# Kernel optimization log

Measured on AMD Instinct MI355X. Metric: run time of the kernel, lower is better.

The kernel has to match this reference:

```python
import jax, jax.numpy as jnp
import numpy as np

N_NODES = 50000
N_EDGES = 1_000_000
N_HYPER = 1024
F_IN = 128
F_EDGE = 64


def setup_inputs() -> dict:
    key = jax.random.key(0)
    ks = jax.random.split(key, 20)
    s = 0.05
    return {
        "x": jax.random.normal(ks[0], (N_NODES, F_IN), jnp.float32),
        "edge_index": jax.random.randint(ks[1], (2, N_EDGES), 0, N_NODES, dtype=jnp.int64),
        "edge_weight": jax.random.uniform(ks[2], (N_EDGES,), jnp.float32),
        "edge_features": jax.random.normal(ks[3], (N_HYPER, F_EDGE), jnp.float32),
        "adj_e": jax.random.uniform(ks[4], (N_HYPER, N_HYPER), jnp.float32) / N_HYPER,
        "T": jax.random.uniform(ks[5], (N_NODES, N_HYPER), jnp.float32) / N_HYPER,
        # HypergraphConvLayer 1: 128 -> 64
        "W1": jax.random.normal(ks[6], (F_IN, 64), jnp.float32) * s,
        "b1": jnp.zeros((64,), jnp.float32),
        # HypergraphConvLayer 2: 64 -> 32
        "W2": jax.random.normal(ks[7], (64, 32), jnp.float32) * s,
        "b2": jnp.zeros((32,), jnp.float32),
        # GraphConvolution (CensNet-style): node 32->32, edge 64->32
        "Wn": jax.random.normal(ks[8], (32, 32), jnp.float32) * s,
        "We": jax.random.normal(ks[9], (F_EDGE, 32), jnp.float32) * s,
        "bg": jnp.zeros((32,), jnp.float32),
        # class_classifier: Linear(32,32) -> ReLU -> Linear(32,2) -> Softmax
        "Wc1": jax.random.normal(ks[10], (32, 32), jnp.float32) * s,
        "bc1": jnp.zeros((32,), jnp.float32),
        "Wc2": jax.random.normal(ks[11], (32, 2), jnp.float32) * s,
        "bc2": jnp.zeros((2,), jnp.float32),
    }


def _hconv(h, W, b, src, dst, edge_weight, num_nodes):
    # linear projection then edge-weighted scatter-add: out[dst] += w * h[src]
    h = h @ W + b
    msg = h[src] * edge_weight[:, None]          # [E, d]
    return jax.ops.segment_sum(msg, dst, num_segments=num_nodes)


def reference(x, edge_index, edge_weight, edge_features, adj_e, T,
              W1, b1, W2, b2, Wn, We, bg, Wc1, bc1, Wc2, bc2):
    n = x.shape[0]
    src, dst = edge_index[0], edge_index[1]

    h = jax.nn.relu(_hconv(x, W1, b1, src, dst, edge_weight, n))   # [N,64]
    h = jax.nn.relu(_hconv(h, W2, b2, src, dst, edge_weight, n))   # [N,32]

    # aggregate_node_features: node_features[dst] += h[src]; / num_edges
    num_edges = edge_index.shape[1]
    node_features = jax.ops.segment_sum(h[src], dst, num_segments=n) / num_edges

    # edge_conv: node linear + incidence-weighted hyperedge convolution
    edge_h = adj_e @ (edge_features @ We)                           # [NE,32]
    shared = jax.nn.relu(node_features @ Wn + T @ edge_h + bg)      # [N,32]

    # class_classifier
    c = jax.nn.relu(shared @ Wc1 + bc1)
    logits = c @ Wc2 + bc2
    return jax.nn.softmax(logits, axis=1)                           # [N,2]
```

## Files before the change

### kernel.cpp

```cpp
#include <hip/hip_runtime.h>
#include <hip/hip_bf16.h>

#define RPB 256

template<int COLS, int K>
__global__ __launch_bounds__(256) void gemm_k(
    const float* __restrict__ X, const float* __restrict__ W,
    const float* __restrict__ bias, float* __restrict__ out,
    int nrows, float scale, int relu_in)
{
    constexpr int CPT = COLS / 8;
    constexpr int KT  = 32;
    constexpr int NKT = K / KT;

    __shared__ float sx[RPB * 36];
    __shared__ float sWT[COLS * 33];

    const int tid = threadIdx.x;
    const int cg  = tid & 7;
    const int rg  = tid >> 3;
    const int r0  = blockIdx.x * RPB;

    float acc[8][CPT];
    #pragma unroll
    for (int r = 0; r < 8; ++r)
        #pragma unroll
        for (int c = 0; c < CPT; ++c) acc[r][c] = 0.f;

    for (int kt = 0; kt < NKT; ++kt) {
        #pragma unroll
        for (int j = 0; j < 8; ++j) {
            int i  = tid + j * 256;
            int r  = i >> 3;
            int k4 = i & 7;
            int gr = r0 + r; if (gr >= nrows) gr = nrows - 1;
            float4 v = *(const float4*)&X[(size_t)gr * K + kt * KT + k4 * 4];
            if (relu_in) {
                v.x = fmaxf(v.x, 0.f); v.y = fmaxf(v.y, 0.f);
                v.z = fmaxf(v.z, 0.f); v.w = fmaxf(v.w, 0.f);
            }
            if (scale != 1.f) { v.x *= scale; v.y *= scale; v.z *= scale; v.w *= scale; }
            *(float4*)&sx[r * 36 + k4 * 4] = v;
        }
        for (int i = tid; i < COLS * KT; i += 256) {
            int kl = i / COLS, c = i % COLS;
            sWT[c * 33 + kl] = W[(size_t)(kt * KT + kl) * COLS + c];
        }
        __syncthreads();

        #pragma unroll
        for (int k4 = 0; k4 < 8; ++k4) {
            float4 a[8];
            #pragma unroll
            for (int r = 0; r < 8; ++r)
                a[r] = *(const float4*)&sx[(r * 32 + rg) * 36 + k4 * 4];
            #pragma unroll
            for (int cc = 0; cc < CPT; ++cc) {
                int c = cg * CPT + cc;
                float w0 = sWT[c * 33 + k4 * 4 + 0];
                float w1 = sWT[c * 33 + k4 * 4 + 1];
                float w2 = sWT[c * 33 + k4 * 4 + 2];
                float w3 = sWT[c * 33 + k4 * 4 + 3];
                #pragma unroll
                for (int r = 0; r < 8; ++r)
                    acc[r][cc] += a[r].x * w0 + a[r].y * w1 + a[r].z * w2 + a[r].w * w3;
            }
        }
        __syncthreads();
    }

    #pragma unroll
    for (int r = 0; r < 8; ++r) {
        int row = r0 + r * 32 + rg;
        if (row < nrows) {
            #pragma unroll
            for (int cc4 = 0; cc4 < CPT / 4; ++cc4) {
                int c = cg * CPT + cc4 * 4;
                float4 o;
                o.x = acc[r][cc4 * 4 + 0] + (bias ? bias[c + 0] : 0.f);
                o.y = acc[r][cc4 * 4 + 1] + (bias ? bias[c + 1] : 0.f);
                o.z = acc[r][cc4 * 4 + 2] + (bias ? bias[c + 2] : 0.f);
                o.w = acc[r][cc4 * 4 + 3] + (bias ? bias[c + 3] : 0.f);
                *(float4*)&out[(size_t)row * COLS + c] = o;
            }
        }
    }
}

__global__ __launch_bounds__(256, 4) void tgemm2_k(
    const float* __restrict__ T, const float* __restrict__ eh,
    float* __restrict__ par, int nrows)
{
    __shared__ float seh[256 * 32];
    const int tid = threadIdx.x;
    const int ks  = blockIdx.y * 256;

    #pragma unroll
    for (int j = 0; j < 8; ++j) {
        int i = tid + j * 256;
        *(float4*)&seh[i * 4] = *(const float4*)&eh[(size_t)ks * 32 + (size_t)i * 4];
    }
    __syncthreads();

    int row = blockIdx.x * 256 + tid;
    int r   = row < nrows ? row : nrows - 1;
    const float* Tp = T + (size_t)r * 1024 + ks;

    float acc[32];
    #pragma unroll
    for (int c = 0; c < 32; ++c) acc[c] = 0.f;

    float4 t[8];
    #pragma unroll
    for (int q = 0; q < 8; ++q) t[q] = *(const float4*)&Tp[q * 4];

    for (int kc = 0; kc < 8; ++kc) {
        float4 tn[8];
        if (kc < 7) {
            #pragma unroll
            for (int q = 0; q < 8; ++q)
                tn[q] = *(const float4*)&Tp[(kc + 1) * 32 + q * 4];
        }
        #pragma unroll
        for (int q = 0; q < 8; ++q) {
            #pragma unroll
            for (int j = 0; j < 4; ++j) {
                float a = (j == 0) ? t[q].x : (j == 1) ? t[q].y : (j == 2) ? t[q].z : t[q].w;
                int k = kc * 32 + q * 4 + j;
                #pragma unroll
                for (int c4 = 0; c4 < 8; ++c4) {
                    float4 w = *(const float4*)&seh[k * 32 + c4 * 4];
                    acc[c4 * 4 + 0] += a * w.x;
                    acc[c4 * 4 + 1] += a * w.y;
                    acc[c4 * 4 + 2] += a * w.z;
                    acc[c4 * 4 + 3] += a * w.w;
                }
            }
        }
        #pragma unroll
        for (int q = 0; q < 8; ++q) t[q] = tn[q];
    }

    if (row < nrows) {
        float* p = par + (size_t)blockIdx.y * nrows * 32 + (size_t)row * 32;
        #pragma unroll
        for (int c4 = 0; c4 < 8; ++c4)
            *(float4*)&p[c4 * 4] = make_float4(acc[c4 * 4 + 0], acc[c4 * 4 + 1],
                                               acc[c4 * 4 + 2], acc[c4 * 4 + 3]);
    }
}

__global__ __launch_bounds__(256) void classify_k(
    const float* __restrict__ par, const float* __restrict__ nfw,
    const float* __restrict__ bg, const float* __restrict__ Wc1,
    const float* __restrict__ bc1, const float* __restrict__ Wc2,
    const float* __restrict__ bc2, float* __restrict__ out, int nrows)
{
    __shared__ float sWc1T[1024];
    __shared__ float sWc2[64];
    __shared__ float sb[66];

    int tid = threadIdx.x;
    for (int i = tid; i < 1024; i += 256)
        sWc1T[(i & 31) * 32 + (i >> 5)] = Wc1[i];
    if (tid < 64) sWc2[tid] = Wc2[tid];
    if (tid < 32)      sb[tid] = bc1[tid];
    else if (tid < 64) sb[tid] = bg[tid - 32];
    else if (tid < 66) sb[tid] = bc2[tid - 64];
    __syncthreads();

    int row = blockIdx.x * 256 + tid;
    if (row >= nrows) return;

    size_t stride = (size_t)nrows * 32;
    float4 sh4[8];
    #pragma unroll
    for (int i4 = 0; i4 < 8; ++i4) {
        const float* base = par + (size_t)row * 32 + i4 * 4;
        float4 v0 = *(const float4*)(base);
        float4 v1 = *(const float4*)(base + stride);
        float4 v2 = *(const float4*)(base + 2 * stride);
        float4 v3 = *(const float4*)(base + 3 * stride);
        float4 nf = *(const float4*)&nfw[(size_t)row * 32 + i4 * 4];
        float4 o;
        o.x = fmaxf(v0.x + v1.x + v2.x + v3.x + nf.x + sb[32 + i4 * 4 + 0], 0.f);
        o.y = fmaxf(v0.y + v1.y + v2.y + v3.y + nf.y + sb[32 + i4 * 4 + 1], 0.f);
        o.z = fmaxf(v0.z + v1.z + v2.z + v3.z + nf.z + sb[32 + i4 * 4 + 2], 0.f);
        o.w = fmaxf(v0.w + v1.w + v2.w + v3.w + nf.w + sb[32 + i4 * 4 + 3], 0.f);
        sh4[i4] = o;
    }

    float l0 = sb[64], l1 = sb[65];
    #pragma unroll
    for (int jj = 0; jj < 32; ++jj) {
        float s = sb[jj];
        #pragma unroll
        for (int i4 = 0; i4 < 8; ++i4) {
            float4 w4 = *(const float4*)&sWc1T[jj * 32 + i4 * 4];
            s += sh4[i4].x * w4.x + sh4[i4].y * w4.y
               + sh4[i4].z * w4.z + sh4[i4].w * w4.w;
        }
        s = fmaxf(s, 0.f);
        l0 += s * sWc2[jj * 2 + 0];
        l1 += s * sWc2[jj * 2 + 1];
    }
    float p0 = 1.f / (1.f + expf(l1 - l0));
    float p1 = 1.f / (1.f + expf(l0 - l1));
    *(float2*)&out[(size_t)row * 2] = make_float2(p0, p1);
}

__global__ void hist_k(const int* __restrict__ dst, int* __restrict__ deg, int E)
{
    int e = blockIdx.x * 256 + threadIdx.x;
    if (e < E) atomicAdd(&deg[dst[e]], 1);
}

__global__ void scan1_k(const int* __restrict__ deg, int* __restrict__ bsum, int N)
{
    __shared__ int s[256];
    int t = threadIdx.x, i = blockIdx.x * 256 + t;
    s[t] = (i < N) ? deg[i] : 0;
    __syncthreads();
    for (int off = 128; off > 0; off >>= 1) {
        if (t < off) s[t] += s[t + off];
        __syncthreads();
    }
    if (t == 0) bsum[blockIdx.x] = s[0];
}

__global__ void scan2_k(const int* __restrict__ bsum, int* __restrict__ boff,
                        int NB, int* __restrict__ rsN)
{
    __shared__ int s[256];
    int t = threadIdx.x;
    int v = (t < NB) ? bsum[t] : 0;
    s[t] = v;
    __syncthreads();
    for (int off = 1; off < 256; off <<= 1) {
        int u = (t >= off) ? s[t - off] : 0;
        __syncthreads();
        s[t] += u;
        __syncthreads();
    }
    if (t < NB) boff[t] = s[t] - v;
    if (t == NB - 1) *rsN = s[t];
}

__global__ void scan3_k(const int* __restrict__ deg, const int* __restrict__ boff,
                        int* __restrict__ rs, int* __restrict__ cur, int N)
{
    __shared__ int s[256];
    int t = threadIdx.x, i = blockIdx.x * 256 + t;
    int v = (i < N) ? deg[i] : 0;
    s[t] = v;
    __syncthreads();
    for (int off = 1; off < 256; off <<= 1) {
        int u = (t >= off) ? s[t - off] : 0;
        __syncthreads();
        s[t] += u;
        __syncthreads();
    }
    if (i < N) {
        int ex = boff[blockIdx.x] + s[t] - v;
        rs[i] = ex;
        cur[i] = ex;
    }
}

__global__ void fill_k(const int* __restrict__ src, const int* __restrict__ dst,
                       const float* __restrict__ ew, int* __restrict__ cur,
                       int2* __restrict__ epk, int E)
{
    int e = blockIdx.x * 256 + threadIdx.x;
    if (e < E) {
        int pos = atomicAdd(&cur[dst[e]], 1);
        epk[pos] = make_int2(src[e], __float_as_int(ew[e]));
    }
}

__global__ __launch_bounds__(256) void gather64_k(
    const float* __restrict__ hp, const int2* __restrict__ epk,
    const int* __restrict__ rs, float* __restrict__ outv, int N)
{
    int t = blockIdx.x * 256 + threadIdx.x;
    if (t >= N * 16) return;
    int n  = t >> 4;
    int ch = t & 15;
    int j0 = rs[n], j1 = rs[n + 1];
    float4 acc = make_float4(0.f, 0.f, 0.f, 0.f);
    for (int j = j0; j < j1; ++j) {
        int2 e = epk[j];
        float w = __int_as_float(e.y);
        float4 v = *(const float4*)&hp[(size_t)e.x * 64 + ch * 4];
        acc.x += v.x * w; acc.y += v.y * w;
        acc.z += v.z * w; acc.w += v.w * w;
    }
    *(float4*)&outv[(size_t)n * 64 + ch * 4] = acc;
}

template<bool WEIGHTED, bool RELU>
__global__ __launch_bounds__(256) void gather32_k(
    const float* __restrict__ hp, const int2* __restrict__ epk,
    const int* __restrict__ rs, float* __restrict__ outv, int N)
{
    int t = blockIdx.x * 256 + threadIdx.x;
    if (t >= N * 8) return;
    int n  = t >> 3;
    int ch = t & 7;
    int j0 = rs[n], j1 = rs[n + 1];
    float4 acc = make_float4(0.f, 0.f, 0.f, 0.f);
    for (int j = j0; j < j1; ++j) {
        int2 e = epk[j];
        float w = WEIGHTED ? __int_as_float(e.y) : 1.f;
        float4 v = *(const float4*)&hp[(size_t)e.x * 32 + ch * 4];
        if (RELU) {
            v.x = fmaxf(v.x, 0.f); v.y = fmaxf(v.y, 0.f);
            v.z = fmaxf(v.z, 0.f); v.w = fmaxf(v.w, 0.f);
        }
        acc.x += v.x * w; acc.y += v.y * w;
        acc.z += v.z * w; acc.w += v.w * w;
    }
    *(float4*)&outv[(size_t)n * 32 + ch * 4] = acc;
}

__global__ void efwe_k(const float* __restrict__ ef, const float* __restrict__ We,
                       float* __restrict__ tmp)
{
    int idx = blockIdx.x * 256 + threadIdx.x;
    int row = idx >> 5, c = idx & 31;
    float s = 0.f;
    #pragma unroll
    for (int k = 0; k < 64; ++k)
        s += ef[row * 64 + k] * We[k * 32 + c];
    tmp[row * 32 + c] = s;
}

__global__ void adjmm_k(const float* __restrict__ adj, const float* __restrict__ tmp,
                        float* __restrict__ edge_h)
{
    int kq     = blockIdx.x & 3;
    int rowblk = blockIdx.x >> 2;
    int r = rowblk * 8 + (threadIdx.x >> 5);
    int c = threadIdx.x & 31;
    float s = 0.f;
    int k0 = kq * 256;
    #pragma unroll 8
    for (int k = k0; k < k0 + 256; ++k)
        s += adj[r * 1024 + k] * tmp[k * 32 + c];
    atomicAdd(&edge_h[r * 32 + c], s);
}

extern "C" void kernel_launch(void* const* d_in, const int* in_sizes, int n_in,
                              void* d_out, int out_size, void* d_ws, size_t ws_size,
                              hipStream_t stream)
{
    const float* x   = (const float*)d_in[0];
    const int*   ei  = (const int*)  d_in[1];
    const float* ew  = (const float*)d_in[2];
    const float* ef  = (const float*)d_in[3];
    const float* adj = (const float*)d_in[4];
    const float* T   = (const float*)d_in[5];
    const float* W1  = (const float*)d_in[6];
    const float* b1  = (const float*)d_in[7];
    const float* W2  = (const float*)d_in[8];
    const float* b2  = (const float*)d_in[9];
    const float* Wn  = (const float*)d_in[10];
    const float* We  = (const float*)d_in[11];
    const float* bg  = (const float*)d_in[12];
    const float* Wc1 = (const float*)d_in[13];
    const float* bc1 = (const float*)d_in[14];
    const float* Wc2 = (const float*)d_in[15];
    const float* bc2 = (const float*)d_in[16];
    float* out = (float*)d_out;

    const int N = in_sizes[0] / 128;
    const int E = in_sizes[1] / 2;
    const int* srcIdx = ei;
    const int* dstIdx = ei + E;

    float* ws = (float*)d_ws;
    size_t o = 0;
    float* h1acc  = ws + o; o += (size_t)N * 64;
    float* h2acc  = ws + o; o += (size_t)N * 32;
    float* nfacc  = ws + o; o += (size_t)N * 32;
    float* edge_h = ws + o; o += 1024 * 32;
    float* tmp    = ws + o; o += 1024 * 32;
    float* nfw    = ws + o; o += (size_t)N * 32;
    float* par    = ws + o; o += (size_t)N * 128;
    float* h1p    = par;
    float* h2p    = par + (size_t)N * 64;
    int2*  epk    = (int2*)(ws + o);  o += (size_t)E * 2;
    int*   deg    = (int*)(ws + o);   o += N;
    int*   rs     = (int*)(ws + o);   o += N + 1;
    int*   cur    = (int*)(ws + o);   o += N + 1;
    int*   bsum   = (int*)(ws + o);   o += 256;
    int*   boff   = (int*)(ws + o);   o += 256;

    const int NB = (N + 255) / 256;

    (void)hipMemsetAsync(deg, 0, (size_t)N * sizeof(int), stream);
    (void)hipMemsetAsync(edge_h, 0, 1024 * 32 * sizeof(float), stream);

    gemm_k<64, 128><<<NB, 256, 0, stream>>>(x, W1, b1, h1p, N, 1.f, 0);

    hist_k<<<(E + 255) / 256, 256, 0, stream>>>(dstIdx, deg, E);
    scan1_k<<<NB, 256, 0, stream>>>(deg, bsum, N);
    scan2_k<<<1, 256, 0, stream>>>(bsum, boff, NB, rs + N);
    scan3_k<<<NB, 256, 0, stream>>>(deg, boff, rs, cur, N);
    fill_k<<<(E + 255) / 256, 256, 0, stream>>>(srcIdx, dstIdx, ew, cur, epk, E);

    gather64_k<<<(N * 16 + 255) / 256, 256, 0, stream>>>(h1p, epk, rs, h1acc, N);

    gemm_k<32, 64><<<NB, 256, 0, stream>>>(h1acc, W2, b2, h2p, N, 1.f, 1);

    gather32_k<true, false><<<(N * 8 + 255) / 256, 256, 0, stream>>>(h2p, epk, rs, h2acc, N);

    gather32_k<false, true><<<(N * 8 + 255) / 256, 256, 0, stream>>>(h2acc, epk, rs, nfacc, N);

    efwe_k<<<128, 256, 0, stream>>>(ef, We, tmp);
    adjmm_k<<<512, 256, 0, stream>>>(adj, tmp, edge_h);

    gemm_k<32, 32><<<NB, 256, 0, stream>>>(nfacc, Wn, nullptr, nfw, N, 1.f / (float)E, 0);

    tgemm2_k<<<dim3(NB, 4), 256, 0, stream>>>(T, edge_h, par, N);

    classify_k<<<NB, 256, 0, stream>>>(par, nfw, bg, Wc1, bc1, Wc2, bc2, out, N);
}
```

Measured before the change: 699.2 us.

## Assign one wavefront per node in gathers and shrink GEMM row tiles

Gather kernels now map one 64-lane wavefront to each destination node, splitting its edge list across lane groups (4 for 64-wide, 8 for 32-wide features) and combining partial sums with xor shuffles. This shortens each thread's serial edge loop and puts more independent loads in flight. The row-wise GEMMs take a rows-per-block template parameter set to 64, giving more blocks and fewer accumulators per thread. The cost is extra shuffle work, idle lanes on low-degree nodes, and more redundant weight tile loads across blocks.

```diff
diff --git a/kernel.cpp b/kernel.cpp
--- a/kernel.cpp
+++ b/kernel.cpp
@@ -1,9 +1,7 @@
 #include <hip/hip_runtime.h>
 #include <hip/hip_bf16.h>
 
-#define RPB 256
-
-template<int COLS, int K>
+template<int COLS, int K, int RPBT>
 __global__ __launch_bounds__(256) void gemm_k(
     const float* __restrict__ X, const float* __restrict__ W,
     const float* __restrict__ bias, float* __restrict__ out,
@@ -12,24 +10,25 @@
     constexpr int CPT = COLS / 8;
     constexpr int KT  = 32;
     constexpr int NKT = K / KT;
-
-    __shared__ float sx[RPB * 36];
+    constexpr int RT  = RPBT / 32;
+
+    __shared__ float sx[RPBT * 36];
     __shared__ float sWT[COLS * 33];
 
     const int tid = threadIdx.x;
     const int cg  = tid & 7;
     const int rg  = tid >> 3;
-    const int r0  = blockIdx.x * RPB;
-
-    float acc[8][CPT];
-    #pragma unroll
-    for (int r = 0; r < 8; ++r)
+    const int r0  = blockIdx.x * RPBT;
+
+    float acc[RT][CPT];
+    #pragma unroll
+    for (int r = 0; r < RT; ++r)
         #pragma unroll
         for (int c = 0; c < CPT; ++c) acc[r][c] = 0.f;
 
     for (int kt = 0; kt < NKT; ++kt) {
         #pragma unroll
-        for (int j = 0; j < 8; ++j) {
+        for (int j = 0; j < RT; ++j) {
             int i  = tid + j * 256;
             int r  = i >> 3;
             int k4 = i & 7;
@@ -50,9 +49,9 @@
 
         #pragma unroll
         for (int k4 = 0; k4 < 8; ++k4) {
-            float4 a[8];
+            float4 a[RT];
             #pragma unroll
-            for (int r = 0; r < 8; ++r)
+            for (int r = 0; r < RT; ++r)
                 a[r] = *(const float4*)&sx[(r * 32 + rg) * 36 + k4 * 4];
             #pragma unroll
             for (int cc = 0; cc < CPT; ++cc) {
@@ -62,7 +61,7 @@
                 float w2 = sWT[c * 33 + k4 * 4 + 2];
                 float w3 = sWT[c * 33 + k4 * 4 + 3];
                 #pragma unroll
-                for (int r = 0; r < 8; ++r)
+                for (int r = 0; r < RT; ++r)
                     acc[r][cc] += a[r].x * w0 + a[r].y * w1 + a[r].z * w2 + a[r].w * w3;
             }
         }
@@ -70,7 +69,7 @@
     }
 
     #pragma unroll
-    for (int r = 0; r < 8; ++r) {
+    for (int r = 0; r < RT; ++r) {
         int row = r0 + r * 32 + rg;
         if (row < nrows) {
             #pragma unroll
@@ -278,38 +277,50 @@
     }
 }
 
-__global__ __launch_bounds__(256) void gather64_k(
+__global__ __launch_bounds__(256) void gather64w_k(
     const float* __restrict__ hp, const int2* __restrict__ epk,
     const int* __restrict__ rs, float* __restrict__ outv, int N)
 {
-    int t = blockIdx.x * 256 + threadIdx.x;
-    if (t >= N * 16) return;
-    int n  = t >> 4;
-    int ch = t & 15;
-    int j0 = rs[n], j1 = rs[n + 1];
+    int wid  = (blockIdx.x * 256 + threadIdx.x) >> 6;
+    if (wid >= N) return;
+    int lane = threadIdx.x & 63;
+    int e4   = lane >> 4;
+    int ch   = lane & 15;
+    int j0 = rs[wid], j1 = rs[wid + 1];
+
     float4 acc = make_float4(0.f, 0.f, 0.f, 0.f);
-    for (int j = j0; j < j1; ++j) {
+    for (int j = j0 + e4; j < j1; j += 4) {
         int2 e = epk[j];
         float w = __int_as_float(e.y);
         float4 v = *(const float4*)&hp[(size_t)e.x * 64 + ch * 4];
         acc.x += v.x * w; acc.y += v.y * w;
         acc.z += v.z * w; acc.w += v.w * w;
     }
-    *(float4*)&outv[(size_t)n * 64 + ch * 4] = acc;
+    #pragma unroll
+    for (int off = 16; off < 64; off <<= 1) {
+        acc.x += __shfl_xor(acc.x, off);
+        acc.y += __shfl_xor(acc.y, off);
+        acc.z += __shfl_xor(acc.z, off);
+        acc.w += __shfl_xor(acc.w, off);
+    }
+    if (e4 == 0)
+        *(float4*)&outv[(size_t)wid * 64 + ch * 4] = acc;
 }
 
 template<bool WEIGHTED, bool RELU>
-__global__ __launch_bounds__(256) void gather32_k(
+__global__ __launch_bounds__(256) void gather32w_k(
     const float* __restrict__ hp, const int2* __restrict__ epk,
     const int* __restrict__ rs, float* __restrict__ outv, int N)
 {
-    int t = blockIdx.x * 256 + threadIdx.x;
-    if (t >= N * 8) return;
-    int n  = t >> 3;
-    int ch = t & 7;
-    int j0 = rs[n], j1 = rs[n + 1];
+    int wid  = (blockIdx.x * 256 + threadIdx.x) >> 6;
+    if (wid >= N) return;
+    int lane = threadIdx.x & 63;
+    int e8   = lane >> 3;
+    int ch   = lane & 7;
+    int j0 = rs[wid], j1 = rs[wid + 1];
+
     float4 acc = make_float4(0.f, 0.f, 0.f, 0.f);
-    for (int j = j0; j < j1; ++j) {
+    for (int j = j0 + e8; j < j1; j += 8) {
         int2 e = epk[j];
         float w = WEIGHTED ? __int_as_float(e.y) : 1.f;
         float4 v = *(const float4*)&hp[(size_t)e.x * 32 + ch * 4];
@@ -320,7 +331,15 @@
         acc.x += v.x * w; acc.y += v.y * w;
         acc.z += v.z * w; acc.w += v.w * w;
     }
-    *(float4*)&outv[(size_t)n * 32 + ch * 4] = acc;
+    #pragma unroll
+    for (int off = 8; off < 64; off <<= 1) {
+        acc.x += __shfl_xor(acc.x, off);
+        acc.y += __shfl_xor(acc.y, off);
+        acc.z += __shfl_xor(acc.z, off);
+        acc.w += __shfl_xor(acc.w, off);
+    }
+    if (e8 == 0)
+        *(float4*)&outv[(size_t)wid * 32 + ch * 4] = acc;
 }
 
 __global__ void efwe_k(const float* __restrict__ ef, const float* __restrict__ We,
@@ -396,12 +415,14 @@
     int*   bsum   = (int*)(ws + o);   o += 256;
     int*   boff   = (int*)(ws + o);   o += 256;
 
-    const int NB = (N + 255) / 256;
+    const int NB  = (N + 255) / 256;
+    const int NBG = (N + 63) / 64;
+    const int NBW = (N * 64 + 255) / 256;
 
     (void)hipMemsetAsync(deg, 0, (size_t)N * sizeof(int), stream);
     (void)hipMemsetAsync(edge_h, 0, 1024 * 32 * sizeof(float), stream);
 
-    gemm_k<64, 128><<<NB, 256, 0, stream>>>(x, W1, b1, h1p, N, 1.f, 0);
+    gemm_k<64, 128, 64><<<NBG, 256, 0, stream>>>(x, W1, b1, h1p, N, 1.f, 0);
 
     hist_k<<<(E + 255) / 256, 256, 0, stream>>>(dstIdx, deg, E);
     scan1_k<<<NB, 256, 0, stream>>>(deg, bsum, N);
@@ -409,18 +430,18 @@
     scan3_k<<<NB, 256, 0, stream>>>(deg, boff, rs, cur, N);
     fill_k<<<(E + 255) / 256, 256, 0, stream>>>(srcIdx, dstIdx, ew, cur, epk, E);
 
-    gather64_k<<<(N * 16 + 255) / 256, 256, 0, stream>>>(h1p, epk, rs, h1acc, N);
-
-    gemm_k<32, 64><<<NB, 256, 0, stream>>>(h1acc, W2, b2, h2p, N, 1.f, 1);
-
-    gather32_k<true, false><<<(N * 8 + 255) / 256, 256, 0, stream>>>(h2p, epk, rs, h2acc, N);
-
-    gather32_k<false, true><<<(N * 8 + 255) / 256, 256, 0, stream>>>(h2acc, epk, rs, nfacc, N);
+    gather64w_k<<<NBW, 256, 0, stream>>>(h1p, epk, rs, h1acc, N);
+
+    gemm_k<32, 64, 64><<<NBG, 256, 0, stream>>>(h1acc, W2, b2, h2p, N, 1.f, 1);
+
+    gather32w_k<true, false><<<NBW, 256, 0, stream>>>(h2p, epk, rs, h2acc, N);
+
+    gather32w_k<false, true><<<NBW, 256, 0, stream>>>(h2acc, epk, rs, nfacc, N);
 
     efwe_k<<<128, 256, 0, stream>>>(ef, We, tmp);
     adjmm_k<<<512, 256, 0, stream>>>(adj, tmp, edge_h);
 
-    gemm_k<32, 32><<<NB, 256, 0, stream>>>(nfacc, Wn, nullptr, nfw, N, 1.f / (float)E, 0);
+    gemm_k<32, 32, 64><<<NBG, 256, 0, stream>>>(nfacc, Wn, nullptr, nfw, N, 1.f / (float)E, 0);
 
     tgemm2_k<<<dim3(NB, 4), 256, 0, stream>>>(T, edge_h, par, N);
 
```

Measured after the change: 702.8 us. About the same (+0.5%).
